# Kernel optimization log

Hardware: AMD Instinct MI355X
Metric: run time of the kernel (lower is better)

## Reference

```python
import jax, jax.numpy as jnp
import numpy as np

T, D, H, C, MAXLEN = 1024, 512, 512, 50257, 150


def setup_inputs() -> dict:
    key = jax.random.key(0)
    ks = iter(jax.random.split(key, 32))
    s = 0.1  # keep gates out of saturation
    def p(shape):
        return jax.random.normal(next(ks), shape, jnp.float32) * s
    return {
        "x": jax.random.normal(next(ks), (T, D), jnp.float32),
        "enc_Wih0": p((2, 4 * H, D)), "enc_Whh0": p((2, 4 * H, H)), "enc_b0": p((2, 4 * H)),
        "enc_Wih1": p((2, 4 * H, 2 * H)), "enc_Whh1": p((2, 4 * H, H)), "enc_b1": p((2, 4 * H)),
        "dec_Wih0": p((2, 4 * H, D)), "dec_Whh0": p((2, 4 * H, H)), "dec_b0": p((2, 4 * H)),
        "dec_Wih1": p((2, 4 * H, 2 * H)), "dec_Whh1": p((2, 4 * H, H)), "dec_b1": p((2, 4 * H)),
        "lin_W": p((C, 2 * H)), "lin_b": p((C,)),
        "emb": p((C, D)),
        "bos": p((D,)),
        "out_max_len": MAXLEN,
    }


def _cell(x, h, c, Wih, Whh, b):
    # PyTorch LSTM gate order: i, f, g, o; b = b_ih + b_hh
    g = Wih @ x + Whh @ h + b
    i, f, gg, o = jnp.split(g, 4)
    c = jax.nn.sigmoid(f) * c + jax.nn.sigmoid(i) * jnp.tanh(gg)
    h = jax.nn.sigmoid(o) * jnp.tanh(c)
    return h, c


def _run_dir(xs, Wih, Whh, b, reverse):
    Hh = Whh.shape[1]
    init = (jnp.zeros((Hh,), xs.dtype), jnp.zeros((Hh,), xs.dtype))
    def step(carry, xt):
        h, c = carry
        h, c = _cell(xt, h, c, Wih, Whh, b)
        return (h, c), h
    (hT, cT), hs = jax.lax.scan(step, init, xs, reverse=reverse)
    return hs, hT, cT  # hs aligned with input order


def _encode(x, layers):
    xs = x  # [T, D]
    h_fin, c_fin = [], []
    for (Wih, Whh, b) in layers:
        hs_f, hf, cf = _run_dir(xs, Wih[0], Whh[0], b[0], False)
        hs_b, hb, cb = _run_dir(xs, Wih[1], Whh[1], b[1], True)
        xs = jnp.concatenate([hs_f, hs_b], axis=-1)  # [T, 2H]
        h_fin.append(jnp.stack([hf, hb]))
        c_fin.append(jnp.stack([cf, cb]))
    return jnp.stack(h_fin), jnp.stack(c_fin)  # [L, 2, H]


def reference(x, enc_Wih0, enc_Whh0, enc_b0, enc_Wih1, enc_Whh1, enc_b1,
              dec_Wih0, dec_Whh0, dec_b0, dec_Wih1, dec_Whh1, dec_b1,
              lin_W, lin_b, emb, bos, out_max_len):
    layers_enc = [(enc_Wih0, enc_Whh0, enc_b0), (enc_Wih1, enc_Whh1, enc_b1)]
    layers_dec = [(dec_Wih0, dec_Whh0, dec_b0), (dec_Wih1, dec_Whh1, dec_b1)]

    h, c = _encode(x, layers_enc)  # [2, 2, H] each

    def dec_step(carry, _):
        buf, h, c = carry
        inp = buf
        nh, nc = [], []
        for l, (Wih, Whh, b) in enumerate(layers_dec):
            hf, cf = _cell(inp, h[l, 0], c[l, 0], Wih[0], Whh[0], b[0])
            hb, cb = _cell(inp, h[l, 1], c[l, 1], Wih[1], Whh[1], b[1])
            inp = jnp.concatenate([hf, hb])  # [2H]
            nh.append(jnp.stack([hf, hb]))
            nc.append(jnp.stack([cf, cb]))
        logits = lin_W @ inp + lin_b          # [C]
        tok = jnp.argmax(logits)              # greedy feedback
        buf = emb[tok]                        # [D]
        return (buf, jnp.stack(nh), jnp.stack(nc)), (logits, tok)

    _, (logits_seq, toks) = jax.lax.scan(dec_step, (bos, h, c), None, length=out_max_len)
    return logits_seq, toks  # [L_out, C], [L_out]
```

## Files before the change

kernel.cpp:

```cpp
#include <hip/hip_runtime.h>
#include <hip/hip_fp16.h>

typedef unsigned int u32;
typedef unsigned short u16;
typedef unsigned long long u64;

#define DEV static __device__ __forceinline__

DEV float sigf(float x){ return 1.0f / (1.0f + expf(-x)); }

DEV u64  ldA64(const u64* p){ return __hip_atomic_load(p, __ATOMIC_RELAXED, __HIP_MEMORY_SCOPE_AGENT); }
DEV void stA64(u64* p, u64 v){ __hip_atomic_store(p, v, __ATOMIC_RELAXED, __HIP_MEMORY_SCOPE_AGENT); }
DEV float ldAf(const float* p){ return __hip_atomic_load(p, __ATOMIC_RELAXED, __HIP_MEMORY_SCOPE_AGENT); }
DEV void stAf(float* p, float v){ __hip_atomic_store(p, v, __ATOMIC_RELAXED, __HIP_MEMORY_SCOPE_AGENT); }
DEV u32  ldA32(const u32* p){ return __hip_atomic_load(p, __ATOMIC_RELAXED, __HIP_MEMORY_SCOPE_AGENT); }

DEV u64 packHV(float h, u32 tag){ return (((u64)__float_as_uint(h)) << 32) | (u64)tag; }
DEV float unpackH(u64 v){ return __uint_as_float((u32)(v >> 32)); }

DEV u64 packKeyT(float v, u32 row, u32 tagv){
  u32 u = __float_as_uint(v);
  u = (u & 0x80000000u) ? ~u : (u | 0x80000000u);
  return (((u64)u) << 32) | ((u64)(0x1FFFFu - row) << 15) | (u64)tagv;
}

DEV float dot8h(const uint4 A, const float4 a, const float4 b){
  const __half2* h = (const __half2*)&A;
  const float2 f0 = __half22float2(h[0]);
  const float2 f1 = __half22float2(h[1]);
  const float2 f2 = __half22float2(h[2]);
  const float2 f3 = __half22float2(h[3]);
  float s;
  s  = f0.x*a.x + f0.y*a.y + f1.x*a.z + f1.y*a.w;
  s += f2.x*b.x + f2.y*b.y + f3.x*b.z + f3.y*b.w;
  return s;
}

DEV float dotrow(const float4 A, const float4 B, const float4 Cc, const float4 D,
                 const float4 q0, const float4 q1, const float4 q2, const float4 q3){
  float s;
  s  = A.x*q0.x + A.y*q0.y + A.z*q0.z + A.w*q0.w;
  s += B.x*q1.x + B.y*q1.y + B.z*q1.z + B.w*q1.w;
  s += Cc.x*q2.x + Cc.y*q2.y + Cc.z*q2.z + Cc.w*q2.w;
  s += D.x*q3.x + D.y*q3.y + D.z*q3.z + D.w*q3.w;
  return s;
}

struct SM {
  float w1s[24576];
  float inpP[1600];
  float linp[1024];
  float srow[256];
  float erow[256];
  float red[8];
  float dots[16];
  float cst0[4];
  float cst1[4];
  u64   wkey[4];
};

template<int CPT> DEV int pidx(int c){ int b = c / CPT; return b * (CPT + 4) + (c - b * CPT); }

template<int CPT, int DIN>
DEV void loadw(float* wreg, const float* Wih, const float* Whh, int jb4){
  const int tid = threadIdx.x, r = tid >> 4, p = tid & 15;
  const int R = 512 * (r >> 2) + jb4 + (r & 3);
  const float* s1 = Wih + (size_t)R * DIN;
  const float* s2 = Whh + (size_t)R * 512;
  #pragma unroll
  for (int k = 0; k < CPT; k += 4){
    const int col = p * CPT + k;
    const float4 v = *(const float4*)((col < DIN) ? (s1 + col) : (s2 + col - DIN));
    wreg[k] = v.x; wreg[k+1] = v.y; wreg[k+2] = v.z; wreg[k+3] = v.w;
  }
}

template<int CPT>
DEV void dot16(const float* wreg, const float* inpP, float* dots){
  const int tid = threadIdx.x, p = tid & 15;
  const float* xi = inpP + p * (CPT + 4);
  float acc = 0.f;
  #pragma unroll
  for (int k = 0; k < CPT; k += 4){
    const float4 xv = *(const float4*)(xi + k);
    acc = fmaf(wreg[k],   xv.x, acc);
    acc = fmaf(wreg[k+1], xv.y, acc);
    acc = fmaf(wreg[k+2], xv.z, acc);
    acc = fmaf(wreg[k+3], xv.w, acc);
  }
  #pragma unroll
  for (int s = 1; s < 16; s <<= 1) acc += __shfl_xor(acc, s, 64);
  if (p == 0) dots[tid >> 4] = acc;
}

DEV void dot16_w1(const float* w1s, const float* inpP, float* dots){
  const int tid = threadIdx.x, p = tid & 15;
  const float* xi = inpP + p * 100;
  float acc = 0.f;
  #pragma unroll
  for (int k = 0; k < 96; k += 4){
    const float4 w4 = *(const float4*)(w1s + (k >> 2) * 1024 + tid * 4);
    const float4 xv = *(const float4*)(xi + k);
    acc = fmaf(w4.x, xv.x, acc);
    acc = fmaf(w4.y, xv.y, acc);
    acc = fmaf(w4.z, xv.z, acc);
    acc = fmaf(w4.w, xv.w, acc);
  }
  #pragma unroll
  for (int s = 1; s < 16; s <<= 1) acc += __shfl_xor(acc, s, 64);
  if (p == 0) dots[tid >> 4] = acc;
}

DEV void gbar_phase(u32* g, u32 ev){
  __syncthreads();
  if (threadIdx.x == 0){
    __hip_atomic_fetch_add(g, 1u, __ATOMIC_RELEASE, __HIP_MEMORY_SCOPE_AGENT);
    const u32 tgt = 256u * ev;
    while (ldA32(g) < tgt) __builtin_amdgcn_s_sleep(8);
    (void)__hip_atomic_fetch_add(g, 0u, __ATOMIC_ACQUIRE, __HIP_MEMORY_SCOPE_AGENT);
    asm volatile("" ::: "memory");
  }
  __syncthreads();
}

template<int DIN, bool WRITE_XS>
DEV void enc_layer(const float* __restrict__ xg, float* __restrict__ xs_out,
                   const float* __restrict__ Wih, const float* __restrict__ Whh,
                   const float* __restrict__ bias,
                   u64* __restrict__ ht, float* __restrict__ hfinL, float* __restrict__ cfinL,
                   const int dir, const int jb4, SM& sm)
{
  constexpr int CPT = (DIN + 512) / 16;
  constexpr int NX  = DIN / 256;
  const int tid = threadIdx.x;
  float wreg[CPT];
  loadw<CPT, DIN>(wreg, Wih + (size_t)dir * 2048 * DIN, Whh + (size_t)dir * 2048 * 512, jb4);
  float b_i = 0.f, b_f = 0.f, b_g = 0.f, b_o = 0.f;
  if (tid < 4){
    const int j = jb4 + tid;
    sm.cst0[tid] = 0.f;
    b_i = bias[dir*2048 +        j];
    b_f = bias[dir*2048 +  512 + j];
    b_g = bias[dir*2048 + 1024 + j];
    b_o = bias[dir*2048 + 1536 + j];
  }
  float xr[NX];
  {
    const int t0 = dir ? 1023 : 0;
    #pragma unroll
    for (int i = 0; i < NX; ++i){
      const int c = tid + 256 * i;
      xr[i] = (DIN == 512) ? xg[(size_t)t0 * DIN + c] : ldAf(xg + (size_t)t0 * DIN + c);
    }
  }
  for (int step = 0; step < 1024; ++step){
    #pragma unroll
    for (int i = 0; i < NX; ++i) sm.inpP[pidx<CPT>(tid + 256 * i)] = xr[i];
    {
      const u64* hp = ht + (step & 1) * 512;
      const u32 want = (u32)step;
      u64 a = ldA64(hp + tid*2), b = ldA64(hp + tid*2 + 1);
      while ((u32)a != want){ __builtin_amdgcn_s_sleep(1); a = ldA64(hp + tid*2); }
      while ((u32)b != want){ __builtin_amdgcn_s_sleep(1); b = ldA64(hp + tid*2 + 1); }
      sm.inpP[pidx<CPT>(DIN + tid*2)]     = unpackH(a);
      sm.inpP[pidx<CPT>(DIN + tid*2 + 1)] = unpackH(b);
    }
    __syncthreads();
    if (step < 1023){
      const int tn = dir ? (1022 - step) : (step + 1);
      #pragma unroll
      for (int i = 0; i < NX; ++i){
        const int c = tid + 256 * i;
        xr[i] = (DIN == 512) ? xg[(size_t)tn * DIN + c] : ldAf(xg + (size_t)tn * DIN + c);
      }
    }
    dot16<CPT>(wreg, sm.inpP, sm.dots);
    __syncthreads();
    if (tid < 4){
      const float gi = sm.dots[tid]      + b_i;
      const float gf = sm.dots[4 + tid]  + b_f;
      const float gg = sm.dots[8 + tid]  + b_g;
      const float go = sm.dots[12 + tid] + b_o;
      const float cc = sigf(gf) * sm.cst0[tid] + sigf(gi) * tanhf(gg);
      const float hh = sigf(go) * tanhf(cc);
      sm.cst0[tid] = cc;
      const int t = dir ? (1023 - step) : step;
      const int j = jb4 + tid;
      stA64(ht + ((step + 1) & 1) * 512 + j, packHV(hh, (u32)(step + 1)));
      if (WRITE_XS) stAf(xs_out + (size_t)t * 1024 + dir * 512 + j, hh);
      if (step == 1023){ stAf(hfinL + dir*512 + j, hh); stAf(cfinL + dir*512 + j, cc); }
    }
    __syncthreads();
  }
}

__global__ void bilstm_init(u32* ws){
  for (u32 i = threadIdx.x; i < 32768u; i += 256u) ws[i] = 0u;
}

__global__ void cvt_lin(const float* __restrict__ w, uint4* __restrict__ o,
                        float* __restrict__ maxw, const int C){
  const int wv = threadIdx.x >> 6, lane = threadIdx.x & 63;
  const int stride = gridDim.x * 4;
  for (int r = blockIdx.x * 4 + wv; r < C; r += stride){
    const float4* src = (const float4*)(w + (size_t)r * 1024) + lane * 4;
    const float4 v0 = src[0], v1 = src[1], v2 = src[2], v3 = src[3];
    uint4 p0, p1;
    __half2 h;
    h = __floats2half2_rn(v0.x, v0.y); p0.x = *(const u32*)&h;
    h = __floats2half2_rn(v0.z, v0.w); p0.y = *(const u32*)&h;
    h = __floats2half2_rn(v1.x, v1.y); p0.z = *(const u32*)&h;
    h = __floats2half2_rn(v1.z, v1.w); p0.w = *(const u32*)&h;
    h = __floats2half2_rn(v2.x, v2.y); p1.x = *(const u32*)&h;
    h = __floats2half2_rn(v2.z, v2.w); p1.y = *(const u32*)&h;
    h = __floats2half2_rn(v3.x, v3.y); p1.z = *(const u32*)&h;
    h = __floats2half2_rn(v3.z, v3.w); p1.w = *(const u32*)&h;
    uint4* dst = o + (size_t)r * 128 + lane * 2;
    dst[0] = p0; dst[1] = p1;
    float m = fmaxf(fmaxf(fmaxf(fabsf(v0.x), fabsf(v0.y)), fmaxf(fabsf(v0.z), fabsf(v0.w))),
                    fmaxf(fmaxf(fabsf(v1.x), fabsf(v1.y)), fmaxf(fabsf(v1.z), fabsf(v1.w))));
    m = fmaxf(m, fmaxf(fmaxf(fabsf(v2.x), fabsf(v2.y)), fmaxf(fabsf(v2.z), fabsf(v2.w))));
    m = fmaxf(m, fmaxf(fmaxf(fabsf(v3.x), fabsf(v3.y)), fmaxf(fabsf(v3.z), fabsf(v3.w))));
    #pragma unroll
    for (int s = 1; s < 64; s <<= 1) m = fmaxf(m, __shfl_xor(m, s, 64));
    if (lane == 0) maxw[r] = m;
  }
}

template<int LINFP16>
__global__ __launch_bounds__(256, 1)
void bilstm_persist(const float* __restrict__ x,
                    const float* __restrict__ eW0, const float* __restrict__ eU0, const float* __restrict__ eb0,
                    const float* __restrict__ eW1, const float* __restrict__ eU1, const float* __restrict__ eb1,
                    const float* __restrict__ dW0, const float* __restrict__ dU0, const float* __restrict__ db0,
                    const float* __restrict__ dW1, const float* __restrict__ dU1, const float* __restrict__ db1,
                    const float* __restrict__ linW, const float* __restrict__ linb,
                    const float* __restrict__ emb, const float* __restrict__ bos,
                    float* __restrict__ out, float* __restrict__ ws, const int L, const int C)
{
  __shared__ SM sm;
  const int w = blockIdx.x;
  const int tid = threadIdx.x;
  const int dir = (w >> 2) & 1;
  const int jb4 = ((w >> 3) * 4 + (w & 3)) * 4;

  u64*  htagE = (u64*)ws;
  u64*  h0t   = htagE + 4096;
  u64*  h1t   = h0t + 2048;
  float* hfin = (float*)(h1t + 2048);
  float* cfin = hfin + 2048;
  u32*  gbar  = (u32*)(cfin + 2048);
  u64*  gkey  = (u64*)((char*)ws + 98304);
  const u16*  linH = (const u16*)((const char*)ws + 131072);
  const float* maxw = (const float*)((const char*)ws + 131072 + (size_t)C * 2048);
  float* xs1  = out;

  enc_layer<512,  true >(x,   xs1,     eW0, eU0, eb0, htagE + (0*2 + dir)*1024, hfin,        cfin,        dir, jb4, sm);
  gbar_phase(gbar, 1);
  enc_layer<1024, false>(xs1, nullptr, eW1, eU1, eb1, htagE + (1*2 + dir)*1024, hfin + 1024, cfin + 1024, dir, jb4, sm);
  gbar_phase(gbar, 2);

  float w0reg[64];
  loadw<64, 512>(w0reg, dW0 + (size_t)dir*2048*512, dU0 + (size_t)dir*2048*512, jb4);
  {
    const int r = tid >> 4, p = tid & 15;
    const int R = 512 * (r >> 2) + jb4 + (r & 3);
    const float* s1 = dW1 + (size_t)dir*2048*1024 + (size_t)R * 1024;
    const float* s2 = dU1 + (size_t)dir*2048*512  + (size_t)R * 512;
    #pragma unroll
    for (int k = 0; k < 96; k += 4){
      const int col = p * 96 + k;
      const float4 v = *(const float4*)((col < 1024) ? (s1 + col) : (s2 + col - 1024));
      *(float4*)(sm.w1s + (k >> 2) * 1024 + tid * 4) = v;
    }
  }

  float b0i=0,b0f=0,b0g=0,b0o=0, b1i=0,b1f=0,b1g=0,b1o=0;
  if (tid < 4){
    const int j = jb4 + tid;
    sm.cst0[tid] = ldAf(&cfin[dir*512 + j]);
    sm.cst1[tid] = ldAf(&cfin[1024 + dir*512 + j]);
    b0i = db0[dir*2048 + j];        b0f = db0[dir*2048 + 512 + j];
    b0g = db0[dir*2048 + 1024 + j]; b0o = db0[dir*2048 + 1536 + j];
    b1i = db1[dir*2048 + j];        b1f = db1[dir*2048 + 512 + j];
    b1g = db1[dir*2048 + 1024 + j]; b1o = db1[dir*2048 + 1536 + j];
  }
  const int rbase = w * 196 + (w < 81 ? w : 81);
  const int rn    = 196 + (w < 81 ? 1 : 0);
  int tok = 0;

  for (int t = 0; t < L; ++t){
    {
      const float* src = (t == 0) ? bos : (emb + (size_t)tok * 512);
      sm.inpP[pidx<64>(tid)]       = src[tid];
      sm.inpP[pidx<64>(tid + 256)] = src[tid + 256];
      if (t == 0){
        sm.inpP[pidx<64>(512 + tid*2)]     = ldAf(&hfin[dir*512 + tid*2]);
        sm.inpP[pidx<64>(512 + tid*2 + 1)] = ldAf(&hfin[dir*512 + tid*2 + 1]);
      } else {
        const u64* hp = h0t + (dir*2 + ((t-1) & 1)) * 512;
        const u32 want = (u32)t;
        u64 a = ldA64(hp + tid*2), b = ldA64(hp + tid*2 + 1);
        while ((u32)a != want){ __builtin_amdgcn_s_sleep(1); a = ldA64(hp + tid*2); }
        while ((u32)b != want){ __builtin_amdgcn_s_sleep(1); b = ldA64(hp + tid*2 + 1); }
        sm.inpP[pidx<64>(512 + tid*2)]     = unpackH(a);
        sm.inpP[pidx<64>(512 + tid*2 + 1)] = unpackH(b);
      }
      __syncthreads();
      dot16<64>(w0reg, sm.inpP, sm.dots);
      __syncthreads();
      if (tid < 4){
        const float gi = sm.dots[tid] + b0i, gf = sm.dots[4+tid] + b0f;
        const float gg = sm.dots[8+tid] + b0g, go = sm.dots[12+tid] + b0o;
        const float cc = sigf(gf) * sm.cst0[tid] + sigf(gi) * tanhf(gg);
        const float hh = sigf(go) * tanhf(cc);
        sm.cst0[tid] = cc;
        stA64(h0t + (dir*2 + (t & 1))*512 + jb4 + tid, packHV(hh, (u32)(t + 1)));
      }
      __syncthreads();
    }

    {
      const u32 want = (u32)(t + 1);
      #pragma unroll
      for (int i = 0; i < 4; ++i){
        const int c = tid + 256 * i;
        const int d = c >> 9, idx = c & 511;
        const u64* hp = h0t + (d*2 + (t & 1)) * 512 + idx;
        u64 v = ldA64(hp);
        while ((u32)v != want){ __builtin_amdgcn_s_sleep(1); v = ldA64(hp); }
        sm.inpP[pidx<96>(c)] = unpackH(v);
      }
      if (t == 0){
        sm.inpP[pidx<96>(1024 + tid*2)]     = ldAf(&hfin[1024 + dir*512 + tid*2]);
        sm.inpP[pidx<96>(1024 + tid*2 + 1)] = ldAf(&hfin[1024 + dir*512 + tid*2 + 1]);
      } else {
        const u64* hq = h1t + (dir*2 + ((t-1) & 1)) * 512;
        const u32 want1 = (u32)t;
        u64 e = ldA64(hq + tid*2), f = ldA64(hq + tid*2 + 1);
        while ((u32)e != want1){ __builtin_amdgcn_s_sleep(1); e = ldA64(hq + tid*2); }
        while ((u32)f != want1){ __builtin_amdgcn_s_sleep(1); f = ldA64(hq + tid*2 + 1); }
        sm.inpP[pidx<96>(1024 + tid*2)]     = unpackH(e);
        sm.inpP[pidx<96>(1024 + tid*2 + 1)] = unpackH(f);
      }
      __syncthreads();
      dot16_w1(sm.w1s, sm.inpP, sm.dots);
      __syncthreads();
      if (tid < 4){
        const float gi = sm.dots[tid] + b1i, gf = sm.dots[4+tid] + b1f;
        const float gg = sm.dots[8+tid] + b1g, go = sm.dots[12+tid] + b1o;
        const float cc = sigf(gf) * sm.cst1[tid] + sigf(gi) * tanhf(gg);
        const float hh = sigf(go) * tanhf(cc);
        sm.cst1[tid] = cc;
        stA64(h1t + (dir*2 + (t & 1))*512 + jb4 + tid, packHV(hh, (u32)(t + 1)));
      }
    }

    {
      const u32 want = (u32)(t + 1);
      float pabs = 0.f;
      #pragma unroll
      for (int i = 0; i < 4; ++i){
        const int c = tid + 256 * i;
        const int d = c >> 9, idx = c & 511;
        const u64* hp = h1t + (d*2 + (t & 1)) * 512 + idx;
        u64 v = ldA64(hp);
        while ((u32)v != want){ __builtin_amdgcn_s_sleep(1); v = ldA64(hp); }
        const float hv = unpackH(v);
        sm.linp[c] = hv;
        pabs += fabsf(hv);
      }
      const int wv = tid >> 6, lane = tid & 63;
      if constexpr (LINFP16){
        #pragma unroll
        for (int s = 1; s < 64; s <<= 1) pabs += __shfl_xor(pabs, s, 64);
        if (lane == 0) sm.red[wv] = pabs;
      }
      __syncthreads();

      const float4* ip4 = (const float4*)(sm.linp + lane * 16);
      const float4 q0 = ip4[0], q1 = ip4[1], q2 = ip4[2], q3 = ip4[3];
      u64 kmax = 0;
      const int rmaxr = rbase + rn - 1;

      if constexpr (LINFP16){
        const float sumabs = sm.red[0] + sm.red[1] + sm.red[2] + sm.red[3];
        const float cErr = sumabs * 7.5e-4f;
        float lb = -1e30f;
        for (int i0 = wv; i0 < rn; i0 += 16){
          const int ia = i0;
          const int ib = (i0 + 4  > rn - 1) ? rn - 1 : i0 + 4;
          const int ic = (i0 + 8  > rn - 1) ? rn - 1 : i0 + 8;
          const int id = (i0 + 12 > rn - 1) ? rn - 1 : i0 + 12;
          const int ra = rbase + ia, rb = rbase + ib, rc = rbase + ic, rd = rbase + id;
          const uint4* pa = (const uint4*)(linH + (size_t)ra * 1024) + lane * 2;
          const uint4* pb = (const uint4*)(linH + (size_t)rb * 1024) + lane * 2;
          const uint4* pc = (const uint4*)(linH + (size_t)rc * 1024) + lane * 2;
          const uint4* pd = (const uint4*)(linH + (size_t)rd * 1024) + lane * 2;
          const uint4 A0 = pa[0], A1 = pa[1];
          const uint4 B0 = pb[0], B1 = pb[1];
          const uint4 C0 = pc[0], C1 = pc[1];
          const uint4 D0 = pd[0], D1 = pd[1];
          float sa = dot8h(A0, q0, q1) + dot8h(A1, q2, q3);
          float sb = dot8h(B0, q0, q1) + dot8h(B1, q2, q3);
          float sc = dot8h(C0, q0, q1) + dot8h(C1, q2, q3);
          float sd = dot8h(D0, q0, q1) + dot8h(D1, q2, q3);
          #pragma unroll
          for (int sh = 1; sh < 64; sh <<= 1){
            sa += __shfl_xor(sa, sh, 64);
            sb += __shfl_xor(sb, sh, 64);
            sc += __shfl_xor(sc, sh, 64);
            sd += __shfl_xor(sd, sh, 64);
          }
          if (lane == 0){
            sa += linb[ra]; sb += linb[rb]; sc += linb[rc]; sd += linb[rd];
            out[(size_t)t * C + ra] = sa;
            out[(size_t)t * C + rb] = sb;
            out[(size_t)t * C + rc] = sc;
            out[(size_t)t * C + rd] = sd;
            const float ea = maxw[ra] * cErr + 1e-4f;
            const float eb = maxw[rb] * cErr + 1e-4f;
            const float ec = maxw[rc] * cErr + 1e-4f;
            const float ed = maxw[rd] * cErr + 1e-4f;
            sm.srow[ia] = sa; sm.erow[ia] = ea;
            sm.srow[ib] = sb; sm.erow[ib] = eb;
            sm.srow[ic] = sc; sm.erow[ic] = ec;
            sm.srow[id] = sd; sm.erow[id] = ed;
            lb = fmaxf(lb, sa - ea); lb = fmaxf(lb, sb - eb);
            lb = fmaxf(lb, sc - ec); lb = fmaxf(lb, sd - ed);
          }
        }
        if (lane == 0) sm.red[4 + wv] = lb;
        __syncthreads();
        const float Lb = fmaxf(fmaxf(sm.red[4], sm.red[5]), fmaxf(sm.red[6], sm.red[7]));
        for (int i = wv; i < rn; i += 4){
          if (sm.srow[i] + sm.erow[i] >= Lb){
            const int row = rbase + i;
            const float4* wp = (const float4*)(linW + (size_t)row * 1024) + lane * 4;
            float s = dotrow(wp[0], wp[1], wp[2], wp[3], q0, q1, q2, q3);
            #pragma unroll
            for (int sh = 1; sh < 64; sh <<= 1) s += __shfl_xor(s, sh, 64);
            if (lane == 0){
              s += linb[row];
              const u64 k = packKeyT(s, (u32)row, (u32)(t + 1));
              if (k > kmax) kmax = k;
            }
          }
        }
      } else {
        for (int i0 = wv; i0 < rn; i0 += 16){
          const int ra = rbase + i0;
          const int rb = (ra + 4  > rmaxr) ? rmaxr : ra + 4;
          const int rc = (ra + 8  > rmaxr) ? rmaxr : ra + 8;
          const int rd = (ra + 12 > rmaxr) ? rmaxr : ra + 12;
          const float ba = linb[ra], bb = linb[rb], bc = linb[rc], bd = linb[rd];
          const float4* pa = (const float4*)(linW + (size_t)ra * 1024) + lane * 4;
          const float4* pb = (const float4*)(linW + (size_t)rb * 1024) + lane * 4;
          const float4* pc = (const float4*)(linW + (size_t)rc * 1024) + lane * 4;
          const float4* pd = (const float4*)(linW + (size_t)rd * 1024) + lane * 4;
          const float4 a0 = pa[0], a1 = pa[1], a2 = pa[2], a3 = pa[3];
          const float4 e0 = pb[0], e1 = pb[1], e2 = pb[2], e3 = pb[3];
          const float4 c0 = pc[0], c1 = pc[1], c2 = pc[2], c3 = pc[3];
          const float4 d0 = pd[0], d1 = pd[1], d2 = pd[2], d3 = pd[3];
          float sa = dotrow(a0,a1,a2,a3, q0,q1,q2,q3);
          float sb = dotrow(e0,e1,e2,e3, q0,q1,q2,q3);
          float sc = dotrow(c0,c1,c2,c3, q0,q1,q2,q3);
          float sd = dotrow(d0,d1,d2,d3, q0,q1,q2,q3);
          #pragma unroll
          for (int sh = 1; sh < 64; sh <<= 1){
            sa += __shfl_xor(sa, sh, 64);
            sb += __shfl_xor(sb, sh, 64);
            sc += __shfl_xor(sc, sh, 64);
            sd += __shfl_xor(sd, sh, 64);
          }
          if (lane == 0){
            sa += ba; sb += bb; sc += bc; sd += bd;
            out[(size_t)t * C + ra] = sa;
            out[(size_t)t * C + rb] = sb;
            out[(size_t)t * C + rc] = sc;
            out[(size_t)t * C + rd] = sd;
            u64 k;
            k = packKeyT(sa, (u32)ra, (u32)(t+1)); if (k > kmax) kmax = k;
            k = packKeyT(sb, (u32)rb, (u32)(t+1)); if (k > kmax) kmax = k;
            k = packKeyT(sc, (u32)rc, (u32)(t+1)); if (k > kmax) kmax = k;
            k = packKeyT(sd, (u32)rd, (u32)(t+1)); if (k > kmax) kmax = k;
          }
        }
      }
      if (lane == 0) sm.wkey[wv] = kmax;
    }

    __syncthreads();
    if (tid == 0){
      u64 k4 = sm.wkey[0];
      if (sm.wkey[1] > k4) k4 = sm.wkey[1];
      if (sm.wkey[2] > k4) k4 = sm.wkey[2];
      if (sm.wkey[3] > k4) k4 = sm.wkey[3];
      stA64(gkey + (size_t)w * 16, k4);
    }
    __syncthreads();
    {
      const u32 wantk = (u32)(t + 1);
      const u64* p = gkey + (size_t)tid * 16;
      u64 kv = ldA64(p);
      while ((u32)(kv & 0x7FFFu) != wantk){ __builtin_amdgcn_s_sleep(1); kv = ldA64(p); }
      #pragma unroll
      for (int s = 1; s < 64; s <<= 1){
        const u64 o = (u64)__shfl_xor((unsigned long long)kv, s, 64);
        if (o > kv) kv = o;
      }
      if ((tid & 63) == 0) sm.wkey[tid >> 6] = kv;
    }
    __syncthreads();
    {
      u64 gk = sm.wkey[0];
      if (sm.wkey[1] > gk) gk = sm.wkey[1];
      if (sm.wkey[2] > gk) gk = sm.wkey[2];
      if (sm.wkey[3] > gk) gk = sm.wkey[3];
      tok = (int)(0x1FFFFu - ((u32)(gk >> 15) & 0x1FFFFu));
      if (w == 0 && tid == 0) out[(size_t)L * C + t] = (float)tok;
    }
  }
}

extern "C" void kernel_launch(void* const* d_in, const int* in_sizes, int n_in,
                              void* d_out, int out_size, void* d_ws, size_t ws_size,
                              hipStream_t stream)
{
  const float* x    = (const float*)d_in[0];
  const float* eW0  = (const float*)d_in[1];
  const float* eU0  = (const float*)d_in[2];
  const float* eb0  = (const float*)d_in[3];
  const float* eW1  = (const float*)d_in[4];
  const float* eU1  = (const float*)d_in[5];
  const float* eb1  = (const float*)d_in[6];
  const float* dW0  = (const float*)d_in[7];
  const float* dU0  = (const float*)d_in[8];
  const float* db0  = (const float*)d_in[9];
  const float* dW1  = (const float*)d_in[10];
  const float* dU1  = (const float*)d_in[11];
  const float* db1  = (const float*)d_in[12];
  const float* linW = (const float*)d_in[13];
  const float* linb = (const float*)d_in[14];
  const float* emb  = (const float*)d_in[15];
  const float* bos  = (const float*)d_in[16];

  const int C = in_sizes[14];
  const int L = out_size / (C + 1);
  const int nlin = in_sizes[13];

  const size_t need = 131072 + (size_t)nlin * 2 + (size_t)C * 4;
  const bool fp16lin = (ws_size >= need);

  hipLaunchKernelGGL(bilstm_init, dim3(1), dim3(256), 0, stream, (u32*)d_ws);
  if (fp16lin){
    hipLaunchKernelGGL(cvt_lin, dim3(2048), dim3(256), 0, stream,
                       linW, (uint4*)((char*)d_ws + 131072),
                       (float*)((char*)d_ws + 131072 + (size_t)C * 2048), C);
    hipLaunchKernelGGL((bilstm_persist<1>), dim3(256), dim3(256), 0, stream,
                       x, eW0, eU0, eb0, eW1, eU1, eb1,
                       dW0, dU0, db0, dW1, dU1, db1,
                       linW, linb, emb, bos,
                       (float*)d_out, (float*)d_ws, L, C);
  } else {
    hipLaunchKernelGGL((bilstm_persist<0>), dim3(256), dim3(256), 0, stream,
                       x, eW0, eU0, eb0, eW1, eU1, eb1,
                       dW0, dU0, db0, dW1, dU1, db1,
                       linW, linb, emb, bos,
                       (float*)d_out, (float*)d_ws, L, C);
  }
}
```

Baseline: 8.860 ms.

## Use int8 screening with global lower bound for vocab projection; overlap encoder input dot

The vocabulary projection now screens rows with int8-quantized weights and activations via sdot4 instead of fp16, using per-row scale and abs-sum metadata to bound the error. The lower bound is exchanged globally across all blocks rather than kept per block, so fewer rows need exact fp32 recomputation. The encoder step starts the input-part dot product before spinning on the hidden-state flags and drops one barrier per step. This adds a second global exchange per decode step, and the int8 bounds must stay correct for argmax exactness.

Measured after the change: 10.37 ms. 17.0% more time.

```diff
diff --git a/kernel.cpp b/kernel.cpp
--- a/kernel.cpp
+++ b/kernel.cpp
@@ -1,5 +1,4 @@
 #include <hip/hip_runtime.h>
-#include <hip/hip_fp16.h>
 
 typedef unsigned int u32;
 typedef unsigned short u16;
@@ -23,17 +22,33 @@
   u = (u & 0x80000000u) ? ~u : (u | 0x80000000u);
   return (((u64)u) << 32) | ((u64)(0x1FFFFu - row) << 15) | (u64)tagv;
 }
-
-DEV float dot8h(const uint4 A, const float4 a, const float4 b){
-  const __half2* h = (const __half2*)&A;
-  const float2 f0 = __half22float2(h[0]);
-  const float2 f1 = __half22float2(h[1]);
-  const float2 f2 = __half22float2(h[2]);
-  const float2 f3 = __half22float2(h[3]);
-  float s;
-  s  = f0.x*a.x + f0.y*a.y + f1.x*a.z + f1.y*a.w;
-  s += f2.x*b.x + f2.y*b.y + f3.x*b.z + f3.y*b.w;
+DEV float unpackKeyF(u64 k){
+  u32 u = (u32)(k >> 32);
+  u = (u & 0x80000000u) ? (u ^ 0x80000000u) : ~u;
+  return __uint_as_float(u);
+}
+
+#if defined(__has_builtin)
+#if __has_builtin(__builtin_amdgcn_sdot4)
+#define HAVE_SDOT4 1
+#endif
+#endif
+DEV int dot4i8(u32 a, u32 b, int acc){
+#ifdef HAVE_SDOT4
+  return __builtin_amdgcn_sdot4((int)a, (int)b, acc, false);
+#else
+  int s = acc;
+  s += ((int)(a << 24) >> 24) * ((int)(b << 24) >> 24);
+  s += ((int)(a << 16) >> 24) * ((int)(b << 16) >> 24);
+  s += ((int)(a <<  8) >> 24) * ((int)(b <<  8) >> 24);
+  s += ((int)(a      ) >> 24) * ((int)(b      ) >> 24);
   return s;
+#endif
+}
+
+DEV int q8c(float v){ int q = (int)rintf(v); return q < -127 ? -127 : (q > 127 ? 127 : q); }
+DEV u32 pk4(int a, int b, int c, int d){
+  return (u32)(a & 255) | ((u32)(b & 255) << 8) | ((u32)(c & 255) << 16) | ((u32)(d & 255) << 24);
 }
 
 DEV float dotrow(const float4 A, const float4 B, const float4 Cc, const float4 D,
@@ -50,8 +65,9 @@
   float w1s[24576];
   float inpP[1600];
   float linp[1024];
-  float srow[256];
-  float erow[256];
+  u32   qhp[256];
+  float srow[200];
+  float erow[200];
   float red[8];
   float dots[16];
   float cst0[4];
@@ -73,6 +89,29 @@
     const float4 v = *(const float4*)((col < DIN) ? (s1 + col) : (s2 + col - DIN));
     wreg[k] = v.x; wreg[k+1] = v.y; wreg[k+2] = v.z; wreg[k+3] = v.w;
   }
+}
+
+template<int CPT, int DIN, bool LOW>
+DEV float dotp_reg(const float* wreg, const float* inpP, float acc){
+  const int p = threadIdx.x & 15;
+  const float* xi = inpP + p * (CPT + 4);
+  #pragma unroll
+  for (int k = 0; k < CPT; k += 4){
+    const int col = p * CPT + k;
+    if ((col < DIN) == LOW){
+      const float4 xv = *(const float4*)(xi + k);
+      acc = fmaf(wreg[k],   xv.x, acc);
+      acc = fmaf(wreg[k+1], xv.y, acc);
+      acc = fmaf(wreg[k+2], xv.z, acc);
+      acc = fmaf(wreg[k+3], xv.w, acc);
+    }
+  }
+  return acc;
+}
+DEV void dred16(float acc, float* dots){
+  #pragma unroll
+  for (int s = 1; s < 16; s <<= 1) acc += __shfl_xor(acc, s, 64);
+  if ((threadIdx.x & 15) == 0) dots[threadIdx.x >> 4] = acc;
 }
 
 template<int CPT>
@@ -88,9 +127,7 @@
     acc = fmaf(wreg[k+2], xv.z, acc);
     acc = fmaf(wreg[k+3], xv.w, acc);
   }
-  #pragma unroll
-  for (int s = 1; s < 16; s <<= 1) acc += __shfl_xor(acc, s, 64);
-  if (p == 0) dots[tid >> 4] = acc;
+  dred16(acc, dots);
 }
 
 DEV void dot16_w1(const float* w1s, const float* inpP, float* dots){
@@ -106,9 +143,7 @@
     acc = fmaf(w4.z, xv.z, acc);
     acc = fmaf(w4.w, xv.w, acc);
   }
-  #pragma unroll
-  for (int s = 1; s < 16; s <<= 1) acc += __shfl_xor(acc, s, 64);
-  if (p == 0) dots[tid >> 4] = acc;
+  dred16(acc, dots);
 }
 
 DEV void gbar_phase(u32* g, u32 ev){
@@ -121,6 +156,35 @@
     asm volatile("" ::: "memory");
   }
   __syncthreads();
+}
+
+DEV u64 exchange(u64* slots, u64 kwave , int w, u32 tagv, SM& sm){
+  const int tid = threadIdx.x;
+  if ((tid & 63) == 0) sm.wkey[tid >> 6] = kwave;
+  __syncthreads();
+  if (tid == 0){
+    u64 k4 = sm.wkey[0];
+    if (sm.wkey[1] > k4) k4 = sm.wkey[1];
+    if (sm.wkey[2] > k4) k4 = sm.wkey[2];
+    if (sm.wkey[3] > k4) k4 = sm.wkey[3];
+    stA64(slots + (size_t)w * 16, k4);
+  }
+  __syncthreads();
+  const u64* p = slots + (size_t)tid * 16;
+  u64 kv = ldA64(p);
+  while ((u32)(kv & 0x7FFFu) != tagv){ __builtin_amdgcn_s_sleep(1); kv = ldA64(p); }
+  #pragma unroll
+  for (int s = 1; s < 64; s <<= 1){
+    const u64 o = (u64)__shfl_xor((unsigned long long)kv, s, 64);
+    if (o > kv) kv = o;
+  }
+  if ((tid & 63) == 0) sm.wkey[tid >> 6] = kv;
+  __syncthreads();
+  u64 gk = sm.wkey[0];
+  if (sm.wkey[1] > gk) gk = sm.wkey[1];
+  if (sm.wkey[2] > gk) gk = sm.wkey[2];
+  if (sm.wkey[3] > gk) gk = sm.wkey[3];
+  return gk;
 }
 
 template<int DIN, bool WRITE_XS>
@@ -156,15 +220,16 @@
   for (int step = 0; step < 1024; ++step){
     #pragma unroll
     for (int i = 0; i < NX; ++i) sm.inpP[pidx<CPT>(tid + 256 * i)] = xr[i];
-    {
-      const u64* hp = ht + (step & 1) * 512;
-      const u32 want = (u32)step;
-      u64 a = ldA64(hp + tid*2), b = ldA64(hp + tid*2 + 1);
-      while ((u32)a != want){ __builtin_amdgcn_s_sleep(1); a = ldA64(hp + tid*2); }
-      while ((u32)b != want){ __builtin_amdgcn_s_sleep(1); b = ldA64(hp + tid*2 + 1); }
-      sm.inpP[pidx<CPT>(DIN + tid*2)]     = unpackH(a);
-      sm.inpP[pidx<CPT>(DIN + tid*2 + 1)] = unpackH(b);
-    }
+    __syncthreads();
+    const u64* hp = ht + (step & 1) * 512;
+    const u32 want = (u32)step;
+    u64 a = ldA64(hp + tid*2);
+    u64 b = ldA64(hp + tid*2 + 1);
+    float acc = dotp_reg<CPT, DIN, true>(wreg, sm.inpP, 0.f);
+    while ((u32)a != want){ __builtin_amdgcn_s_sleep(1); a = ldA64(hp + tid*2); }
+    while ((u32)b != want){ __builtin_amdgcn_s_sleep(1); b = ldA64(hp + tid*2 + 1); }
+    sm.inpP[pidx<CPT>(DIN + tid*2)]     = unpackH(a);
+    sm.inpP[pidx<CPT>(DIN + tid*2 + 1)] = unpackH(b);
     __syncthreads();
     if (step < 1023){
       const int tn = dir ? (1022 - step) : (step + 1);
@@ -174,7 +239,8 @@
         xr[i] = (DIN == 512) ? xg[(size_t)tn * DIN + c] : ldAf(xg + (size_t)tn * DIN + c);
       }
     }
-    dot16<CPT>(wreg, sm.inpP, sm.dots);
+    acc = dotp_reg<CPT, DIN, false>(wreg, sm.inpP, acc);
+    dred16(acc, sm.dots);
     __syncthreads();
     if (tid < 4){
       const float gi = sm.dots[tid]      + b_i;
@@ -190,44 +256,45 @@
       if (WRITE_XS) stAf(xs_out + (size_t)t * 1024 + dir * 512 + j, hh);
       if (step == 1023){ stAf(hfinL + dir*512 + j, hh); stAf(cfinL + dir*512 + j, cc); }
     }
-    __syncthreads();
   }
 }
 
 __global__ void bilstm_init(u32* ws){
-  for (u32 i = threadIdx.x; i < 32768u; i += 256u) ws[i] = 0u;
-}
-
-__global__ void cvt_lin(const float* __restrict__ w, uint4* __restrict__ o,
-                        float* __restrict__ maxw, const int C){
+  for (u32 i = threadIdx.x; i < 49152u; i += 256u) ws[i] = 0u;
+}
+
+__global__ void cvt_q8(const float* __restrict__ w, uint4* __restrict__ q8,
+                       float* __restrict__ meta, const int C){
   const int wv = threadIdx.x >> 6, lane = threadIdx.x & 63;
   const int stride = gridDim.x * 4;
   for (int r = blockIdx.x * 4 + wv; r < C; r += stride){
     const float4* src = (const float4*)(w + (size_t)r * 1024) + lane * 4;
     const float4 v0 = src[0], v1 = src[1], v2 = src[2], v3 = src[3];
-    uint4 p0, p1;
-    __half2 h;
-    h = __floats2half2_rn(v0.x, v0.y); p0.x = *(const u32*)&h;
-    h = __floats2half2_rn(v0.z, v0.w); p0.y = *(const u32*)&h;
-    h = __floats2half2_rn(v1.x, v1.y); p0.z = *(const u32*)&h;
-    h = __floats2half2_rn(v1.z, v1.w); p0.w = *(const u32*)&h;
-    h = __floats2half2_rn(v2.x, v2.y); p1.x = *(const u32*)&h;
-    h = __floats2half2_rn(v2.z, v2.w); p1.y = *(const u32*)&h;
-    h = __floats2half2_rn(v3.x, v3.y); p1.z = *(const u32*)&h;
-    h = __floats2half2_rn(v3.z, v3.w); p1.w = *(const u32*)&h;
-    uint4* dst = o + (size_t)r * 128 + lane * 2;
-    dst[0] = p0; dst[1] = p1;
     float m = fmaxf(fmaxf(fmaxf(fabsf(v0.x), fabsf(v0.y)), fmaxf(fabsf(v0.z), fabsf(v0.w))),
                     fmaxf(fmaxf(fabsf(v1.x), fabsf(v1.y)), fmaxf(fabsf(v1.z), fabsf(v1.w))));
     m = fmaxf(m, fmaxf(fmaxf(fabsf(v2.x), fabsf(v2.y)), fmaxf(fabsf(v2.z), fabsf(v2.w))));
     m = fmaxf(m, fmaxf(fmaxf(fabsf(v3.x), fabsf(v3.y)), fmaxf(fabsf(v3.z), fabsf(v3.w))));
     #pragma unroll
     for (int s = 1; s < 64; s <<= 1) m = fmaxf(m, __shfl_xor(m, s, 64));
-    if (lane == 0) maxw[r] = m;
-  }
-}
-
-template<int LINFP16>
+    const float inv = (m > 1e-30f) ? (127.0f / m) : 0.0f;
+    const float sw = m * (1.0f / 127.0f);
+    const int qa0 = q8c(v0.x*inv), qa1 = q8c(v0.y*inv), qa2 = q8c(v0.z*inv), qa3 = q8c(v0.w*inv);
+    const int qb0 = q8c(v1.x*inv), qb1 = q8c(v1.y*inv), qb2 = q8c(v1.z*inv), qb3 = q8c(v1.w*inv);
+    const int qc0 = q8c(v2.x*inv), qc1 = q8c(v2.y*inv), qc2 = q8c(v2.z*inv), qc3 = q8c(v2.w*inv);
+    const int qd0 = q8c(v3.x*inv), qd1 = q8c(v3.y*inv), qd2 = q8c(v3.z*inv), qd3 = q8c(v3.w*inv);
+    uint4 st;
+    st.x = pk4(qa0,qa1,qa2,qa3); st.y = pk4(qb0,qb1,qb2,qb3);
+    st.z = pk4(qc0,qc1,qc2,qc3); st.w = pk4(qd0,qd1,qd2,qd3);
+    q8[(size_t)r * 64 + lane] = st;
+    float sq = (float)(abs(qa0)+abs(qa1)+abs(qa2)+abs(qa3)+abs(qb0)+abs(qb1)+abs(qb2)+abs(qb3)
+                     + abs(qc0)+abs(qc1)+abs(qc2)+abs(qc3)+abs(qd0)+abs(qd1)+abs(qd2)+abs(qd3));
+    #pragma unroll
+    for (int s = 1; s < 64; s <<= 1) sq += __shfl_xor(sq, s, 64);
+    if (lane == 0){ meta[2*r] = sw; meta[2*r+1] = sq; }
+  }
+}
+
+template<int LINQ8>
 __global__ __launch_bounds__(256, 1)
 void bilstm_persist(const float* __restrict__ x,
                     const float* __restrict__ eW0, const float* __restrict__ eU0, const float* __restrict__ eb0,
@@ -250,9 +317,10 @@
   float* hfin = (float*)(h1t + 2048);
   float* cfin = hfin + 2048;
   u32*  gbar  = (u32*)(cfin + 2048);
-  u64*  gkey  = (u64*)((char*)ws + 98304);
-  const u16*  linH = (const u16*)((const char*)ws + 131072);
-  const float* maxw = (const float*)((const char*)ws + 131072 + (size_t)C * 2048);
+  u64*  gkeyA = (u64*)((char*)ws + 131072);
+  u64*  gkeyB = (u64*)((char*)ws + 163840);
+  const float* meta = (const float*)((const char*)ws + 196608);
+  const uint4* q8u  = (const uint4*)((const char*)ws + 602112);
   float* xs1  = out;
 
   enc_layer<512,  true >(x,   xs1,     eW0, eU0, eb0, htagE + (0*2 + dir)*1024, hfin,        cfin,        dir, jb4, sm);
@@ -356,9 +424,10 @@
       }
     }
 
+    const int wv = tid >> 6, lane = tid & 63;
     {
       const u32 want = (u32)(t + 1);
-      float pabs = 0.f;
+      float pm = 0.f;
       #pragma unroll
       for (int i = 0; i < 4; ++i){
         const int c = tid + 256 * i;
@@ -368,60 +437,69 @@
         while ((u32)v != want){ __builtin_amdgcn_s_sleep(1); v = ldA64(hp); }
         const float hv = unpackH(v);
         sm.linp[c] = hv;
-        pabs += fabsf(hv);
-      }
-      const int wv = tid >> 6, lane = tid & 63;
-      if constexpr (LINFP16){
+        pm = fmaxf(pm, fabsf(hv));
+      }
+
+      if constexpr (LINQ8){
         #pragma unroll
-        for (int s = 1; s < 64; s <<= 1) pabs += __shfl_xor(pabs, s, 64);
-        if (lane == 0) sm.red[wv] = pabs;
-      }
-      __syncthreads();
-
-      const float4* ip4 = (const float4*)(sm.linp + lane * 16);
-      const float4 q0 = ip4[0], q1 = ip4[1], q2 = ip4[2], q3 = ip4[3];
-      u64 kmax = 0;
-      const int rmaxr = rbase + rn - 1;
-
-      if constexpr (LINFP16){
-        const float sumabs = sm.red[0] + sm.red[1] + sm.red[2] + sm.red[3];
-        const float cErr = sumabs * 7.5e-4f;
-        float lb = -1e30f;
+        for (int s = 1; s < 64; s <<= 1) pm = fmaxf(pm, __shfl_xor(pm, s, 64));
+        if (lane == 0) sm.red[wv] = pm;
+        __syncthreads();
+        const float maxh = fmaxf(fmaxf(sm.red[0], sm.red[1]), fmaxf(sm.red[2], sm.red[3]));
+        const float inv_sh = (maxh > 1e-30f) ? (127.0f / maxh) : 0.0f;
+        const float sh = maxh * (1.0f / 127.0f);
+        {
+          const float4 hv = *(const float4*)(sm.linp + 4 * tid);
+          const int q0 = q8c(hv.x * inv_sh), q1 = q8c(hv.y * inv_sh);
+          const int q2 = q8c(hv.z * inv_sh), q3 = q8c(hv.w * inv_sh);
+          sm.qhp[tid] = pk4(q0, q1, q2, q3);
+          float sq = (float)(abs(q0) + abs(q1) + abs(q2) + abs(q3));
+          #pragma unroll
+          for (int s = 1; s < 64; s <<= 1) sq += __shfl_xor(sq, s, 64);
+          if (lane == 0) sm.red[4 + wv] = sq;
+        }
+        __syncthreads();
+        const float Sqh = sm.red[4] + sm.red[5] + sm.red[6] + sm.red[7];
+        const u32 qh0 = sm.qhp[lane*4], qh1 = sm.qhp[lane*4+1];
+        const u32 qh2 = sm.qhp[lane*4+2], qh3 = sm.qhp[lane*4+3];
+        float lb = -3.0e38f;
         for (int i0 = wv; i0 < rn; i0 += 16){
           const int ia = i0;
-          const int ib = (i0 + 4  > rn - 1) ? rn - 1 : i0 + 4;
-          const int ic = (i0 + 8  > rn - 1) ? rn - 1 : i0 + 8;
-          const int id = (i0 + 12 > rn - 1) ? rn - 1 : i0 + 12;
-          const int ra = rbase + ia, rb = rbase + ib, rc = rbase + ic, rd = rbase + id;
-          const uint4* pa = (const uint4*)(linH + (size_t)ra * 1024) + lane * 2;
-          const uint4* pb = (const uint4*)(linH + (size_t)rb * 1024) + lane * 2;
-          const uint4* pc = (const uint4*)(linH + (size_t)rc * 1024) + lane * 2;
-          const uint4* pd = (const uint4*)(linH + (size_t)rd * 1024) + lane * 2;
-          const uint4 A0 = pa[0], A1 = pa[1];
-          const uint4 B0 = pb[0], B1 = pb[1];
-          const uint4 C0 = pc[0], C1 = pc[1];
-          const uint4 D0 = pd[0], D1 = pd[1];
-          float sa = dot8h(A0, q0, q1) + dot8h(A1, q2, q3);
-          float sb = dot8h(B0, q0, q1) + dot8h(B1, q2, q3);
-          float sc = dot8h(C0, q0, q1) + dot8h(C1, q2, q3);
-          float sd = dot8h(D0, q0, q1) + dot8h(D1, q2, q3);
+          const int ib = (i0+4  > rn-1) ? rn-1 : i0+4;
+          const int ic = (i0+8  > rn-1) ? rn-1 : i0+8;
+          const int id = (i0+12 > rn-1) ? rn-1 : i0+12;
+          const int ra = rbase+ia, rb = rbase+ib, rc = rbase+ic, rd = rbase+id;
+          const float2 Ma = *(const float2*)(meta + 2*ra);
+          const float2 Mb = *(const float2*)(meta + 2*rb);
+          const float2 Mc = *(const float2*)(meta + 2*rc);
+          const float2 Md = *(const float2*)(meta + 2*rd);
+          const uint4 wa = q8u[(size_t)ra*64 + lane];
+          const uint4 wb = q8u[(size_t)rb*64 + lane];
+          const uint4 wc = q8u[(size_t)rc*64 + lane];
+          const uint4 wd = q8u[(size_t)rd*64 + lane];
+          int da = dot4i8(wa.x,qh0, dot4i8(wa.y,qh1, dot4i8(wa.z,qh2, dot4i8(wa.w,qh3, 0))));
+          int db = dot4i8(wb.x,qh0, dot4i8(wb.y,qh1, dot4i8(wb.z,qh2, dot4i8(wb.w,qh3, 0))));
+          int dc = dot4i8(wc.x,qh0, dot4i8(wc.y,qh1, dot4i8(wc.z,qh2, dot4i8(wc.w,qh3, 0))));
+          int dd = dot4i8(wd.x,qh0, dot4i8(wd.y,qh1, dot4i8(wd.z,qh2, dot4i8(wd.w,qh3, 0))));
           #pragma unroll
-          for (int sh = 1; sh < 64; sh <<= 1){
-            sa += __shfl_xor(sa, sh, 64);
-            sb += __shfl_xor(sb, sh, 64);
-            sc += __shfl_xor(sc, sh, 64);
-            sd += __shfl_xor(sd, sh, 64);
+          for (int s = 1; s < 64; s <<= 1){
+            da += __shfl_xor(da, s, 64);
+            db += __shfl_xor(db, s, 64);
+            dc += __shfl_xor(dc, s, 64);
+            dd += __shfl_xor(dd, s, 64);
           }
           if (lane == 0){
-            sa += linb[ra]; sb += linb[rb]; sc += linb[rc]; sd += linb[rd];
-            out[(size_t)t * C + ra] = sa;
-            out[(size_t)t * C + rb] = sb;
-            out[(size_t)t * C + rc] = sc;
-            out[(size_t)t * C + rd] = sd;
-            const float ea = maxw[ra] * cErr + 1e-4f;
-            const float eb = maxw[rb] * cErr + 1e-4f;
-            const float ec = maxw[rc] * cErr + 1e-4f;
-            const float ed = maxw[rd] * cErr + 1e-4f;
+            const float ca = Ma.x * sh, cb = Mb.x * sh, cc2 = Mc.x * sh, cd = Md.x * sh;
+            const float sa = ca * (float)da + linb[ra];
+            const float sb = cb * (float)db + linb[rb];
+            const float sc = cc2 * (float)dc + linb[rc];
+            const float sd = cd * (float)dd + linb[rd];
+            const float ea = ca * (0.5f*(Ma.y + Sqh) + 256.0f) * 1.0002f + 1e-4f;
+            const float eb = cb * (0.5f*(Mb.y + Sqh) + 256.0f) * 1.0002f + 1e-4f;
+            const float ec = cc2 * (0.5f*(Mc.y + Sqh) + 256.0f) * 1.0002f + 1e-4f;
+            const float ed = cd * (0.5f*(Md.y + Sqh) + 256.0f) * 1.0002f + 1e-4f;
+            out[(size_t)t*C + ra] = sa; out[(size_t)t*C + rb] = sb;
+            out[(size_t)t*C + rc] = sc; out[(size_t)t*C + rd] = sd;
             sm.srow[ia] = sa; sm.erow[ia] = ea;
             sm.srow[ib] = sb; sm.erow[ib] = eb;
             sm.srow[ic] = sc; sm.erow[ic] = ec;
@@ -430,24 +508,34 @@
             lb = fmaxf(lb, sc - ec); lb = fmaxf(lb, sd - ed);
           }
         }
-        if (lane == 0) sm.red[4 + wv] = lb;
-        __syncthreads();
-        const float Lb = fmaxf(fmaxf(sm.red[4], sm.red[5]), fmaxf(sm.red[6], sm.red[7]));
+        const u64 gkA = exchange(gkeyA, packKeyT(lb, 0u, (u32)(t+1)), w, (u32)(t+1), sm);
+        const float Lb = unpackKeyF(gkA);
+        u64 kwB = packKeyT(-3.0e38f, 0x1FFFFu, (u32)(t+1));
+        const float4* ip4 = (const float4*)(sm.linp + lane * 16);
+        const float4 q0f = ip4[0], q1f = ip4[1], q2f = ip4[2], q3f = ip4[3];
         for (int i = wv; i < rn; i += 4){
           if (sm.srow[i] + sm.erow[i] >= Lb){
             const int row = rbase + i;
             const float4* wp = (const float4*)(linW + (size_t)row * 1024) + lane * 4;
-            float s = dotrow(wp[0], wp[1], wp[2], wp[3], q0, q1, q2, q3);
+            float s = dotrow(wp[0], wp[1], wp[2], wp[3], q0f, q1f, q2f, q3f);
             #pragma unroll
-            for (int sh = 1; sh < 64; sh <<= 1) s += __shfl_xor(s, sh, 64);
+            for (int sh2 = 1; sh2 < 64; sh2 <<= 1) s += __shfl_xor(s, sh2, 64);
             if (lane == 0){
               s += linb[row];
-              const u64 k = packKeyT(s, (u32)row, (u32)(t + 1));
-              if (k > kmax) kmax = k;
+              const u64 k = packKeyT(s, (u32)row, (u32)(t+1));
+              if (k > kwB) kwB = k;
             }
           }
         }
+        const u64 gkB = exchange(gkeyB, kwB, w, (u32)(t+1), sm);
+        tok = (int)(0x1FFFFu - ((u32)(gkB >> 15) & 0x1FFFFu));
+        if (w == 0 && tid == 0) out[(size_t)L * C + t] = (float)tok;
       } else {
+        __syncthreads();
+        const float4* ip4 = (const float4*)(sm.linp + lane * 16);
+        const float4 q0 = ip4[0], q1 = ip4[1], q2 = ip4[2], q3 = ip4[3];
+        u64 kmax = packKeyT(-3.0e38f, 0x1FFFFu, (u32)(t+1));
+        const int rmaxr = rbase + rn - 1;
         for (int i0 = wv; i0 < rn; i0 += 16){
           const int ra = rbase + i0;
           const int rb = (ra + 4  > rmaxr) ? rmaxr : ra + 4;
@@ -458,14 +546,10 @@
           const float4* pb = (const float4*)(linW + (size_t)rb * 1024) + lane * 4;
           const float4* pc = (const float4*)(linW + (size_t)rc * 1024) + lane * 4;
           const float4* pd = (const float4*)(linW + (size_t)rd * 1024) + lane * 4;
-          const float4 a0 = pa[0], a1 = pa[1], a2 = pa[2], a3 = pa[3];
-          const float4 e0 = pb[0], e1 = pb[1], e2 = pb[2], e3 = pb[3];
-          const float4 c0 = pc[0], c1 = pc[1], c2 = pc[2], c3 = pc[3];
-          const float4 d0 = pd[0], d1 = pd[1], d2 = pd[2], d3 = pd[3];
-          float sa = dotrow(a0,a1,a2,a3, q0,q1,q2,q3);
-          float sb = dotrow(e0,e1,e2,e3, q0,q1,q2,q3);
-          float sc = dotrow(c0,c1,c2,c3, q0,q1,q2,q3);
-          float sd = dotrow(d0,d1,d2,d3, q0,q1,q2,q3);
+          float sa = dotrow(pa[0],pa[1],pa[2],pa[3], q0,q1,q2,q3);
+          float sb = dotrow(pb[0],pb[1],pb[2],pb[3], q0,q1,q2,q3);
+          float sc = dotrow(pc[0],pc[1],pc[2],pc[3], q0,q1,q2,q3);
+          float sd = dotrow(pd[0],pd[1],pd[2],pd[3], q0,q1,q2,q3);
           #pragma unroll
           for (int sh = 1; sh < 64; sh <<= 1){
             sa += __shfl_xor(sa, sh, 64);
@@ -486,39 +570,10 @@
             k = packKeyT(sd, (u32)rd, (u32)(t+1)); if (k > kmax) kmax = k;
           }
         }
-      }
-      if (lane == 0) sm.wkey[wv] = kmax;
-    }
-
-    __syncthreads();
-    if (tid == 0){
-      u64 k4 = sm.wkey[0];
-      if (sm.wkey[1] > k4) k4 = sm.wkey[1];
-      if (sm.wkey[2] > k4) k4 = sm.wkey[2];
-      if (sm.wkey[3] > k4) k4 = sm.wkey[3];
-      stA64(gkey + (size_t)w * 16, k4);
-    }
-    __syncthreads();
-    {
-      const u32 wantk = (u32)(t + 1);
-      const u64* p = gkey + (size_t)tid * 16;
-      u64 kv = ldA64(p);
-      while ((u32)(kv & 0x7FFFu) != wantk){ __builtin_amdgcn_s_sleep(1); kv = ldA64(p); }
-      #pragma unroll
-      for (int s = 1; s < 64; s <<= 1){
-        const u64 o = (u64)__shfl_xor((unsigned long long)kv, s, 64);
-        if (o > kv) kv = o;
-      }
-      if ((tid & 63) == 0) sm.wkey[tid >> 6] = kv;
-    }
-    __syncthreads();
-    {
-      u64 gk = sm.wkey[0];
-      if (sm.wkey[1] > gk) gk = sm.wkey[1];
-      if (sm.wkey[2] > gk) gk = sm.wkey[2];
-      if (sm.wkey[3] > gk) gk = sm.wkey[3];
-      tok = (int)(0x1FFFFu - ((u32)(gk >> 15) & 0x1FFFFu));
-      if (w == 0 && tid == 0) out[(size_t)L * C + t] = (float)tok;
+        const u64 gkB = exchange(gkeyB, kmax, w, (u32)(t+1), sm);
+        tok = (int)(0x1FFFFu - ((u32)(gkB >> 15) & 0x1FFFFu));
+        if (w == 0 && tid == 0) out[(size_t)L * C + t] = (float)tok;
+      }
     }
   }
 }
@@ -547,16 +602,15 @@
 
   const int C = in_sizes[14];
   const int L = out_size / (C + 1);
-  const int nlin = in_sizes[13];
-
-  const size_t need = 131072 + (size_t)nlin * 2 + (size_t)C * 4;
-  const bool fp16lin = (ws_size >= need);
+
+  const size_t need = 602112 + (size_t)C * 1024;
+  const bool q8 = (ws_size >= need);
 
   hipLaunchKernelGGL(bilstm_init, dim3(1), dim3(256), 0, stream, (u32*)d_ws);
-  if (fp16lin){
-    hipLaunchKernelGGL(cvt_lin, dim3(2048), dim3(256), 0, stream,
-                       linW, (uint4*)((char*)d_ws + 131072),
-                       (float*)((char*)d_ws + 131072 + (size_t)C * 2048), C);
+  if (q8){
+    hipLaunchKernelGGL(cvt_q8, dim3(2048), dim3(256), 0, stream,
+                       linW, (uint4*)((char*)d_ws + 602112),
+                       (float*)((char*)d_ws + 196608), C);
     hipLaunchKernelGGL((bilstm_persist<1>), dim3(256), dim3(256), 0, stream,
                        x, eW0, eU0, eb0, eW1, eU1, eb1,
                        dW0, dU0, db0, dW1, dU1, db1,
```
